# Optimization experiments

Measured on AMD Instinct MI355X. Metric: run time of the kernel, lower is better.

## Reference

```python
import jax, jax.numpy as jnp
import numpy as np

B, T, C, H = 4, 2048, 1024, 16
D = C // H  # head dim = 64


def setup_inputs() -> dict:
    key = jax.random.key(0)
    ks = jax.random.split(key, 6)
    s = 1.0 / np.sqrt(C)
    return {
        "x": jax.random.normal(ks[0], (B, T, C), dtype=jnp.float32),
        "Wk": jax.random.uniform(ks[1], (C, C), jnp.float32, -s, s),
        "Wq": jax.random.uniform(ks[2], (C, C), jnp.float32, -s, s),
        "Wv": jax.random.uniform(ks[3], (C, C), jnp.float32, -s, s),
        "Wp": jax.random.uniform(ks[4], (C, C), jnp.float32, -s, s),
        "bp": jax.random.uniform(ks[5], (C,), jnp.float32, -s, s),
    }


def reference(x, Wk, Wq, Wv, Wp, bp):
    # nn.Linear applies y = x @ W.T
    def split_heads(y):  # [B,T,C] -> [B,H,T,D]
        return y.reshape(B, T, H, D).transpose(0, 2, 1, 3)

    k = split_heads(x @ Wk.T)
    q = split_heads(x @ Wq.T)
    v = split_heads(x @ Wv.T)
    scale = 1.0 / np.sqrt(D)
    aff = jnp.einsum("bhtd,bhsd->bhts", q, k) * scale  # [B,H,T,T]
    aff = jax.nn.softmax(aff, axis=-1)
    out = jnp.einsum("bhts,bhsd->bhtd", aff, v)  # [B,H,T,D]
    out = out.transpose(0, 2, 1, 3).reshape(B, T, C)
    return out @ Wp.T + bp
```

## Files before the change

### kernel.cpp

```cpp
#include <hip/hip_runtime.h>
#include <stdint.h>

typedef __bf16 bf16_t;
typedef bf16_t bf16x2 __attribute__((ext_vector_type(2)));
typedef bf16_t bf16x8 __attribute__((ext_vector_type(8)));
typedef float f32x4 __attribute__((ext_vector_type(4)));
typedef float f32x16 __attribute__((ext_vector_type(16)));
typedef unsigned short u16;
typedef u16 u16x8 __attribute__((ext_vector_type(8)));
typedef u16 u16x4 __attribute__((ext_vector_type(4)));
typedef unsigned int u32;
typedef u32 u32x2 __attribute__((ext_vector_type(2)));
typedef u32 u32x4v __attribute__((ext_vector_type(4)));

__device__ __forceinline__ u16 f2b(float f) {
  uint32_t u = __builtin_bit_cast(uint32_t, f);
  u += 0x7fffu + ((u >> 16) & 1u);
  return (u16)(u >> 16);
}

__device__ __forceinline__ u32 pkbf(float lo, float hi) {
  bf16x2 t = {(__bf16)lo, (__bf16)hi};
  return __builtin_bit_cast(u32, t);
}

__device__ __forceinline__ void gl_lds16(const void* g, void* l) {
  __builtin_amdgcn_global_load_lds(
      (const __attribute__((address_space(1))) uint32_t*)(uintptr_t)g,
      (__attribute__((address_space(3))) uint32_t*)(uintptr_t)l, 16, 0, 0);
}

__global__ void cast5_bf16(const float* __restrict__ x, const float* __restrict__ a,
                           const float* __restrict__ b, const float* __restrict__ c,
                           const float* __restrict__ d,
                           u16* __restrict__ xb, u16* __restrict__ wb) {
  const int y = blockIdx.y;
  const float* srcs[5] = {x, a, b, c, d};
  const float* src = srcs[y];
  u16* dp = (y == 0) ? xb : wb + (size_t)(y - 1) * 1024 * 1024;
  const int n8 = (y == 0) ? 1048576 : 131072;
  int i = blockIdx.x * blockDim.x + threadIdx.x;
  int stride = gridDim.x * blockDim.x;
  for (; i < n8; i += stride) {
    float4 p = ((const float4*)src)[2 * i];
    float4 q = ((const float4*)src)[2 * i + 1];
    u16x8 o;
    o[0] = f2b(p.x); o[1] = f2b(p.y); o[2] = f2b(p.z); o[3] = f2b(p.w);
    o[4] = f2b(q.x); o[5] = f2b(q.y); o[6] = f2b(q.z); o[7] = f2b(q.w);
    ((u16x8*)dp)[i] = o;
  }
}

__global__ __launch_bounds__(256, 2)
void gemm_qkv(const u16* __restrict__ A, const u16* __restrict__ W3,
              u16* __restrict__ qb, u16* __restrict__ kb2, u16* __restrict__ vtb,
              float qscale) {
  __shared__ u16 As[128 * 64];
  __shared__ u16 Bs[128 * 64];
  const int tid  = threadIdx.x;
  const int lane = tid & 63;
  const int w    = tid >> 6;
  const int wm   = w >> 1, wn = w & 1;
  const int g    = lane >> 4, c = lane & 15;
  const int id   = blockIdx.x;
  const int wg   = (id & 7) * 192 + (id >> 3);
  const int which = wg >> 9;
  const int rem   = wg & 511;
  const int n0    = (rem & 7) * 128;
  const int m0    = (rem >> 3) * 128;
  const u16* Wt = W3 + (size_t)which * 1024 * 1024;

  f32x4 acc[4][4] = {};

  const int srow = tid >> 3;
  const int sslx = (tid & 7) ^ (srow & 7);
  const u16* gA = A  + (size_t)(m0 + srow) * 1024 + sslx * 8;
  const u16* gB = Wt + (size_t)(n0 + srow) * 1024 + sslx * 8;
  char* lA = (char*)As + w * 1024;
  char* lB = (char*)Bs + w * 1024;
  const int cx = c & 7;

#pragma unroll 1
  for (int kt = 0; kt < 1024; kt += 64) {
    __syncthreads();
#pragma unroll
    for (int j = 0; j < 4; ++j) {
      gl_lds16(gA + kt + (size_t)j * 32 * 1024, lA + j * 4096);
      gl_lds16(gB + kt + (size_t)j * 32 * 1024, lB + j * 4096);
    }
    __syncthreads();
#pragma unroll
    for (int ks = 0; ks < 2; ++ks) {
      bf16x8 af[4], bfr[4];
#pragma unroll
      for (int mi = 0; mi < 4; ++mi)
        af[mi] = *(const bf16x8*)((const char*)As + (wm * 64 + mi * 16 + c) * 128 +
                                  (((ks * 4 + g) ^ cx) << 4));
#pragma unroll
      for (int ni = 0; ni < 4; ++ni)
        bfr[ni] = *(const bf16x8*)((const char*)Bs + (wn * 64 + ni * 16 + c) * 128 +
                                   (((ks * 4 + g) ^ cx) << 4));
#pragma unroll
      for (int mi = 0; mi < 4; ++mi)
#pragma unroll
        for (int ni = 0; ni < 4; ++ni)
          acc[mi][ni] = __builtin_amdgcn_mfma_f32_16x16x32_bf16(af[mi], bfr[ni], acc[mi][ni], 0, 0, 0);
    }
  }

  const int rowb = m0 + wm * 64;
  const int colb = n0 + wn * 64;

  if (which <= 1) {
    u16* outb = (which == 0) ? qb : kb2;
    const float scale = (which == 0) ? qscale : 1.0f;
#pragma unroll
    for (int mi = 0; mi < 4; ++mi)
#pragma unroll
      for (int ni = 0; ni < 4; ++ni) {
        size_t base = (size_t)(rowb + mi * 16 + g * 4) * 1024 + (colb + ni * 16 + c);
#pragma unroll
        for (int r = 0; r < 4; ++r)
          outb[base + (size_t)r * 1024] = f2b(acc[mi][ni][r] * scale);
      }
  } else {
#pragma unroll
    for (int mi = 0; mi < 4; ++mi) {
      int row = rowb + mi * 16 + g * 4;
      int bb = row >> 11, tl = row & 2047;
#pragma unroll
      for (int ni = 0; ni < 4; ++ni) {
        int col = colb + ni * 16 + c;
        u16x4 pk;
#pragma unroll
        for (int r = 0; r < 4; ++r) pk[r] = f2b(acc[mi][ni][r]);
        *(u16x4*)(vtb + ((size_t)(bb * 1024 + col)) * 2048 + tl) = pk;
      }
    }
  }
}

__global__ __launch_bounds__(256, 2)
void gemm_out(const u16* __restrict__ A, const u16* __restrict__ Wt,
              float* __restrict__ outf, const float* __restrict__ bias) {
  __shared__ u16 As[128 * 64];
  __shared__ u16 Bs[128 * 64];
  const int tid  = threadIdx.x;
  const int lane = tid & 63;
  const int w    = tid >> 6;
  const int wm   = w >> 1, wn = w & 1;
  const int g    = lane >> 4, c = lane & 15;
  const int id   = blockIdx.x;
  const int wg   = (id & 7) * 64 + (id >> 3);
  const int n0   = (wg & 7) * 128;
  const int m0   = (wg >> 3) * 128;

  f32x4 acc[4][4] = {};

  const int srow = tid >> 3;
  const int sslx = (tid & 7) ^ (srow & 7);
  const u16* gA = A  + (size_t)(m0 + srow) * 1024 + sslx * 8;
  const u16* gB = Wt + (size_t)(n0 + srow) * 1024 + sslx * 8;
  char* lA = (char*)As + w * 1024;
  char* lB = (char*)Bs + w * 1024;
  const int cx = c & 7;

#pragma unroll 1
  for (int kt = 0; kt < 1024; kt += 64) {
    __syncthreads();
#pragma unroll
    for (int j = 0; j < 4; ++j) {
      gl_lds16(gA + kt + (size_t)j * 32 * 1024, lA + j * 4096);
      gl_lds16(gB + kt + (size_t)j * 32 * 1024, lB + j * 4096);
    }
    __syncthreads();
#pragma unroll
    for (int ks = 0; ks < 2; ++ks) {
      bf16x8 af[4], bfr[4];
#pragma unroll
      for (int mi = 0; mi < 4; ++mi)
        af[mi] = *(const bf16x8*)((const char*)As + (wm * 64 + mi * 16 + c) * 128 +
                                  (((ks * 4 + g) ^ cx) << 4));
#pragma unroll
      for (int ni = 0; ni < 4; ++ni)
        bfr[ni] = *(const bf16x8*)((const char*)Bs + (wn * 64 + ni * 16 + c) * 128 +
                                   (((ks * 4 + g) ^ cx) << 4));
#pragma unroll
      for (int mi = 0; mi < 4; ++mi)
#pragma unroll
        for (int ni = 0; ni < 4; ++ni)
          acc[mi][ni] = __builtin_amdgcn_mfma_f32_16x16x32_bf16(af[mi], bfr[ni], acc[mi][ni], 0, 0, 0);
    }
  }

  const int rowb = m0 + wm * 64;
  const int colb = n0 + wn * 64;
#pragma unroll
  for (int ni = 0; ni < 4; ++ni) {
    int col = colb + ni * 16 + c;
    float bv = bias[col];
#pragma unroll
    for (int mi = 0; mi < 4; ++mi) {
      size_t base = (size_t)(rowb + mi * 16 + g * 4) * 1024 + col;
#pragma unroll
      for (int r = 0; r < 4; ++r)
        outf[base + (size_t)r * 1024] = acc[mi][ni][r] + bv;
    }
  }
}

__global__ __launch_bounds__(256, 2)
void attn_fused(const u16* __restrict__ qb, const u16* __restrict__ kb,
                const u16* __restrict__ vt, u16* __restrict__ ob) {
  __shared__ u16 KV[2][4096];

  const int bh = blockIdx.x;
  const int qt = blockIdx.y;
  const int b  = bh >> 4, h = bh & 15;
  const int tid  = threadIdx.x;
  const int lane = tid & 63;
  const int w    = tid >> 6;
  const int l31  = lane & 31, g32 = lane >> 5;

  const int r  = tid >> 3, sl = tid & 7;
  const u16* kgp = kb + (size_t)(b * 2048 + r) * 1024 + h * 64 + sl * 8;
  const u16* vgp = vt + (size_t)(bh * 64 + r) * 2048 + sl * 8;
  const int wb = r * 128 + ((sl * 16) ^ ((r & 7) << 4));
  char* lK = (char*)&KV[0][0];
  char* lV = (char*)&KV[1][0];

  const int qrow0 = b * 2048 + qt * 256 + w * 64;
  bf16x8 qf[2][4];
#pragma unroll
  for (int q2 = 0; q2 < 2; ++q2)
#pragma unroll
    for (int dc = 0; dc < 4; ++dc)
      qf[q2][dc] = *(const bf16x8*)(qb + (size_t)(qrow0 + q2 * 32 + l31) * 1024 +
                                    h * 64 + dc * 16 + g32 * 8);

  f32x16 Oa[2][2] = {};
  float lp[2] = {0.f, 0.f};

  const int xorv = (l31 & 7) << 4;
  const int rowb = l31 * 128;

  uint4 pK0 = *(const uint4*)(kgp);
  uint4 pK1 = *(const uint4*)(kgp + (size_t)32 * 1024);
  uint4 pV0 = *(const uint4*)(vgp);
  uint4 pV1 = *(const uint4*)(vgp + (size_t)32 * 2048);

#pragma unroll 1
  for (int step = 0; step < 32; ++step) {
    __syncthreads();
    *(uint4*)(lK + wb)        = pK0;
    *(uint4*)(lK + wb + 4096) = pK1;
    *(uint4*)(lV + wb)        = pV0;
    *(uint4*)(lV + wb + 4096) = pV1;
    __syncthreads();

    if (step + 1 < 32) {
      const int s1 = (step + 1) * 64;
      pK0 = *(const uint4*)(kgp + (size_t)s1 * 1024);
      pK1 = *(const uint4*)(kgp + (size_t)(s1 + 32) * 1024);
      pV0 = *(const uint4*)(vgp + s1);
      pV1 = *(const uint4*)(vgp + s1 + (size_t)32 * 2048);
    }

    const char* kt  = (const char*)&KV[0][0];
    const char* vtl = (const char*)&KV[1][0];

#pragma unroll
    for (int kb2 = 0; kb2 < 2; ++kb2) {
      bf16x8 kf[4];
#pragma unroll
      for (int dc = 0; dc < 4; ++dc)
        kf[dc] = *(const bf16x8*)(kt + kb2 * 4096 + rowb + ((dc * 32 + g32 * 16) ^ xorv));
      bf16x8 vf[2][2];
#pragma unroll
      for (int db = 0; db < 2; ++db)
#pragma unroll
        for (int ck = 0; ck < 2; ++ck)
          vf[db][ck] = *(const bf16x8*)(vtl + db * 4096 + rowb +
                                        (((kb2 * 2 + ck) * 32 + g32 * 16) ^ xorv));

#pragma unroll
      for (int q2 = 0; q2 < 2; ++q2) {
        f32x16 S = {};
#pragma unroll
        for (int dc = 0; dc < 4; ++dc)
          S = __builtin_amdgcn_mfma_f32_32x32x16_bf16(kf[dc], qf[q2][dc], S, 0, 0, 0);

        float p[16];
#pragma unroll
        for (int rr = 0; rr < 16; ++rr) p[rr] = __builtin_amdgcn_exp2f(S[rr]);
        float s01 = (p[0] + p[1]) + (p[2] + p[3]);
        float s02 = (p[4] + p[5]) + (p[6] + p[7]);
        float s03 = (p[8] + p[9]) + (p[10] + p[11]);
        float s04 = (p[12] + p[13]) + (p[14] + p[15]);
        lp[q2] += (s01 + s02) + (s03 + s04);

        u32 w0 = pkbf(p[0], p[1]),   w1 = pkbf(p[2], p[3]);
        u32 w2 = pkbf(p[4], p[5]),   w3 = pkbf(p[6], p[7]);
        u32 w4 = pkbf(p[8], p[9]),   w5 = pkbf(p[10], p[11]);
        u32 w6 = pkbf(p[12], p[13]), w7 = pkbf(p[14], p[15]);
        u32x2 sA = __builtin_amdgcn_permlane32_swap(w0, w2, false, false);
        u32x2 sB = __builtin_amdgcn_permlane32_swap(w1, w3, false, false);
        u32x2 sC = __builtin_amdgcn_permlane32_swap(w4, w6, false, false);
        u32x2 sD = __builtin_amdgcn_permlane32_swap(w5, w7, false, false);
        u32x4v q0 = {sA[0], sB[0], sA[1], sB[1]};
        u32x4v q1 = {sC[0], sD[0], sC[1], sD[1]};
        bf16x8 pb0 = __builtin_bit_cast(bf16x8, q0);
        bf16x8 pb1 = __builtin_bit_cast(bf16x8, q1);

#pragma unroll
        for (int db = 0; db < 2; ++db) {
          Oa[q2][db] = __builtin_amdgcn_mfma_f32_32x32x16_bf16(vf[db][0], pb0, Oa[q2][db], 0, 0, 0);
          Oa[q2][db] = __builtin_amdgcn_mfma_f32_32x32x16_bf16(vf[db][1], pb1, Oa[q2][db], 0, 0, 0);
        }
      }
    }
  }

#pragma unroll
  for (int q2 = 0; q2 < 2; ++q2) {
    float v = lp[q2];
    v += __shfl_xor(v, 32);
    float rinv = 1.0f / v;
    const size_t rb = (size_t)(qrow0 + q2 * 32 + l31) * 1024 + h * 64;
#pragma unroll
    for (int db = 0; db < 2; ++db)
#pragma unroll
      for (int pr = 0; pr < 8; ++pr) {
        int reg = 2 * pr;
        int d0  = (reg & 3) + 8 * (reg >> 2) + 4 * g32 + db * 32;
        u32 pk = pkbf(Oa[q2][db][reg] * rinv, Oa[q2][db][reg + 1] * rinv);
        *(u32*)(ob + rb + d0) = pk;
      }
  }
}

extern "C" void kernel_launch(void* const* d_in, const int* in_sizes, int n_in,
                              void* d_out, int out_size, void* d_ws, size_t ws_size,
                              hipStream_t stream) {
  const float* x  = (const float*)d_in[0];
  const float* Wk = (const float*)d_in[1];
  const float* Wq = (const float*)d_in[2];
  const float* Wv = (const float*)d_in[3];
  const float* Wp = (const float*)d_in[4];
  const float* bp = (const float*)d_in[5];
  float* out = (float*)d_out;

  const size_t MC = (size_t)8192 * 1024;
  u16* xb  = (u16*)d_ws;
  u16* qb  = xb + MC;
  u16* kb2 = qb + MC;
  u16* vtb = kb2 + MC;
  u16* wqb = vtb + MC;
  u16* wpb = wqb + (size_t)3 * 1024 * 1024;
  u16* ob  = xb;

  cast5_bf16<<<dim3(512, 5), 256, 0, stream>>>(x, Wq, Wk, Wv, Wp, xb, wqb);

  const float qscale = 0.125f * 1.44269504088896340736f;
  gemm_qkv<<<1536, 256, 0, stream>>>(xb, wqb, qb, kb2, vtb, qscale);

  attn_fused<<<dim3(64, 8), 256, 0, stream>>>(qb, kb2, vtb, ob);

  gemm_out<<<512, 256, 0, stream>>>(ob, wpb, out, bp);
}
```

Before: 168.9 us.

## Load K/V tiles directly global-to-LDS and drop register prefetch

Replaces the register-staged K/V tile loads (global to VGPR, then ds_write) with direct global-to-LDS loads via a gl_lds16 helper. The XOR swizzle moves to the global source column so each wave writes contiguous LDS. This removes the LDS-write instructions and the prefetch registers. It also drops the software prefetch of the next tile, so load latency is no longer overlapped with compute unless occupancy hides it.

```diff
diff --git a/kernel.cpp b/kernel.cpp
--- a/kernel.cpp
+++ b/kernel.cpp
@@ -222,12 +222,12 @@
   const int w    = tid >> 6;
   const int l31  = lane & 31, g32 = lane >> 5;
 
-  const int r  = tid >> 3, sl = tid & 7;
-  const u16* kgp = kb + (size_t)(b * 2048 + r) * 1024 + h * 64 + sl * 8;
-  const u16* vgp = vt + (size_t)(bh * 64 + r) * 2048 + sl * 8;
-  const int wb = r * 128 + ((sl * 16) ^ ((r & 7) << 4));
-  char* lK = (char*)&KV[0][0];
-  char* lV = (char*)&KV[1][0];
+  const int r  = tid >> 3;
+  const int sx = (tid & 7) ^ (r & 7);
+  const u16* kgs = kb + (size_t)(b * 2048 + r) * 1024 + h * 64 + sx * 8;
+  const u16* vgs = vt + (size_t)(bh * 64 + r) * 2048 + sx * 8;
+  char* lK = (char*)&KV[0][0] + w * 1024;
+  char* lV = (char*)&KV[1][0] + w * 1024;
 
   const int qrow0 = b * 2048 + qt * 256 + w * 64;
   bf16x8 qf[2][4];
@@ -244,27 +244,15 @@
   const int xorv = (l31 & 7) << 4;
   const int rowb = l31 * 128;
 
-  uint4 pK0 = *(const uint4*)(kgp);
-  uint4 pK1 = *(const uint4*)(kgp + (size_t)32 * 1024);
-  uint4 pV0 = *(const uint4*)(vgp);
-  uint4 pV1 = *(const uint4*)(vgp + (size_t)32 * 2048);
-
 #pragma unroll 1
   for (int step = 0; step < 32; ++step) {
-    __syncthreads();
-    *(uint4*)(lK + wb)        = pK0;
-    *(uint4*)(lK + wb + 4096) = pK1;
-    *(uint4*)(lV + wb)        = pV0;
-    *(uint4*)(lV + wb + 4096) = pV1;
-    __syncthreads();
-
-    if (step + 1 < 32) {
-      const int s1 = (step + 1) * 64;
-      pK0 = *(const uint4*)(kgp + (size_t)s1 * 1024);
-      pK1 = *(const uint4*)(kgp + (size_t)(s1 + 32) * 1024);
-      pV0 = *(const uint4*)(vgp + s1);
-      pV1 = *(const uint4*)(vgp + s1 + (size_t)32 * 2048);
-    }
+    const int s0 = step * 64;
+    __syncthreads();
+    gl_lds16(kgs + (size_t)s0 * 1024,        lK);
+    gl_lds16(kgs + (size_t)(s0 + 32) * 1024, lK + 4096);
+    gl_lds16(vgs + s0,                       lV);
+    gl_lds16(vgs + s0 + (size_t)32 * 2048,   lV + 4096);
+    __syncthreads();
 
     const char* kt  = (const char*)&KV[0][0];
     const char* vtl = (const char*)&KV[1][0];
```

Measured after the change: 168.3 us, median of 2. About the same (-0.3%).
